# Performance work log

Measured on AMD Instinct MI355X. Metric: run time of the kernel, lower is better.

Reference implementation:

```python
import jax, jax.numpy as jnp
import numpy as np
import math

B, SQ, SK, DQ, DK = 16, 2048, 2048, 1024, 1024

def setup_inputs() -> dict:
    key = jax.random.key(0)
    ks = jax.random.split(key, 6)
    return {
        "bert_feature": jax.random.normal(ks[0], (B, SQ, DQ), dtype=jnp.float32),
        "knowledge_feature": jax.random.normal(ks[1], (B, SK, DK), dtype=jnp.float32),
        "w1_w": jax.random.normal(ks[2], (DK, DQ), dtype=jnp.float32) * 0.02,
        "w1_b": jax.random.normal(ks[3], (DK,), dtype=jnp.float32) * 0.02,
        "w2_w": jax.random.normal(ks[4], (DQ, DQ + DK), dtype=jnp.float32) * 0.02,
        "w2_b": jax.random.normal(ks[5], (DQ,), dtype=jnp.float32) * 0.02,
    }

def reference(bert_feature, knowledge_feature, w1_w, w1_b, w2_w, w2_b):
    d_k = knowledge_feature.shape[-1]
    # w1 projection: [B, Sq, d_q] -> [B, Sq, d_k]
    bf = jnp.einsum('bqd,kd->bqk', bert_feature, w1_w) + w1_b
    # scaled dot-product attention with knowledge as K and V
    scores = jnp.einsum('bqd,bkd->bqk', bf, knowledge_feature) / math.sqrt(d_k)
    attn = jax.nn.softmax(scores, axis=-1)
    output = jnp.einsum('bqk,bkd->bqd', attn, knowledge_feature)
    # concat + fusion linear: [B, Sq, d_q + d_k] -> [B, Sq, d_q]
    fused = jnp.concatenate([bert_feature, output], axis=-1)
    return jnp.einsum('bqf,of->bqo', fused, w2_w) + w2_b
```

## Files before the change

kernel.cpp:

```cpp
#include <hip/hip_runtime.h>

typedef __attribute__((ext_vector_type(8))) short s16x8;
typedef __attribute__((ext_vector_type(8))) unsigned short u16x8;
typedef __attribute__((ext_vector_type(4))) unsigned short u16x4;
typedef __attribute__((ext_vector_type(4))) float f32x4;

__device__ inline float bf2f(unsigned short h) {
  union { unsigned int u; float f; } x; x.u = ((unsigned int)h) << 16; return x.f;
}
__device__ inline unsigned short f2bf(float f) {
  union { float f; unsigned int u; } x; x.f = f;
  unsigned int u = x.u;
  return (unsigned short)((u + 0x7fffu + ((u >> 16) & 1u)) >> 16);
}

__global__ __launch_bounds__(256) void cvt_bf16(const float* __restrict__ in,
                                                unsigned short* __restrict__ out,
                                                long long n, int shift, int ldo) {
  long long i = (long long)blockIdx.x * 256 + threadIdx.x;
  long long stride = (long long)gridDim.x * 256;
  long long nchunks = n >> 3;
  for (; i < nchunks; i += stride) {
    long long e = i << 3;
    long long r = e >> shift;
    int c = (int)(e & ((1LL << shift) - 1));
    const float4* p = (const float4*)(in + e);
    float4 f0 = p[0], f1 = p[1];
    u16x8 u;
    u[0] = f2bf(f0.x); u[1] = f2bf(f0.y); u[2] = f2bf(f0.z); u[3] = f2bf(f0.w);
    u[4] = f2bf(f1.x); u[5] = f2bf(f1.y); u[6] = f2bf(f1.z); u[7] = f2bf(f1.w);
    *(u16x8*)&out[r * (long long)ldo + c] = u;
  }
}

__global__ __launch_bounds__(256) void transpose_bf16(const unsigned short* __restrict__ in,
                                                      unsigned short* __restrict__ out,
                                                      int rows, int cols) {
  __shared__ unsigned short tile[64][72];
  long long zoff = (long long)blockIdx.z * rows * cols;
  const unsigned short* src = in + zoff;
  unsigned short* dst = out + zoff;
  int k0 = blockIdx.x * 64, d0 = blockIdx.y * 64;
  int t = threadIdx.x;
  int rr = t >> 4;
  int cc = (t & 15) * 4;
#pragma unroll
  for (int i = 0; i < 4; ++i) {
    int k = rr + i * 16;
    u16x4 v = *(const u16x4*)&src[(long long)(k0 + k) * cols + d0 + cc];
    *(u16x4*)&tile[k][cc] = v;
  }
  __syncthreads();
#pragma unroll
  for (int i = 0; i < 4; ++i) {
    int d = rr + i * 16;
    u16x4 v;
#pragma unroll
    for (int j = 0; j < 4; ++j) v[j] = tile[cc + j][d];
    *(u16x4*)&dst[(long long)(d0 + d) * rows + k0 + cc] = v;
  }
}

__global__ __launch_bounds__(256) void softmax_rows(unsigned short* __restrict__ P) {
  int w = threadIdx.x >> 6, l = threadIdx.x & 63;
  long long row = (long long)blockIdx.x * 4 + w;
  unsigned short* p = P + row * 2048;
  float v[32];
  float m = -1e30f;
#pragma unroll
  for (int c = 0; c < 4; ++c) {
    u16x8 u = *(const u16x8*)&p[c * 512 + l * 8];
#pragma unroll
    for (int j = 0; j < 8; ++j) { v[c * 8 + j] = bf2f(u[j]); m = fmaxf(m, v[c * 8 + j]); }
  }
#pragma unroll
  for (int s = 32; s; s >>= 1) m = fmaxf(m, __shfl_xor(m, s));
  float sum = 0.f;
#pragma unroll
  for (int i = 0; i < 32; ++i) { v[i] = __expf(v[i] - m); sum += v[i]; }
#pragma unroll
  for (int s = 32; s; s >>= 1) sum += __shfl_xor(sum, s);
  float r = 1.0f / sum;
#pragma unroll
  for (int c = 0; c < 4; ++c) {
    u16x8 u;
#pragma unroll
    for (int j = 0; j < 8; ++j) u[j] = f2bf(v[c * 8 + j] * r);
    *(u16x8*)&p[c * 512 + l * 8] = u;
  }
}

template <bool OUT_BF16, bool HAS_BIAS>
__global__ __launch_bounds__(512, 1) void gemm256(
    const unsigned short* __restrict__ A, const unsigned short* __restrict__ Bt,
    void* __restrict__ C, const float* __restrict__ bias,
    int K, int lda, int ldb, int ldc,
    long long sA, long long sB, long long sC, float scale,
    int gx, int gy) {
  __shared__ char lds[131072];
  const int t = threadIdx.x;
  const int l = t & 63, w = t >> 6;
  const int wm = w >> 2, wn = w & 3;

  const int nwg = gridDim.x;
  const int id = blockIdx.x;
  const int sid = (id & 7) * (nwg >> 3) + (id >> 3);
  const int bx = sid % gx;
  const int rem = sid / gx;
  const int by = rem % gy;
  const int bz = rem / gy;

  A += (long long)bz * sA;
  Bt += (long long)bz * sB;
  const long long m0 = (long long)by * 256;
  const long long n0 = (long long)bx * 256;

  const int srow = t >> 2;
  const int sk = (((t & 3) * 16) ^ (((t >> 3) & 3) << 4)) >> 1;
  const unsigned short* ga0 = A + (m0 + srow) * lda + sk;
  const unsigned short* ga1 = A + (m0 + 128 + srow) * lda + sk;
  const unsigned short* gb0 = Bt + (n0 + srow) * ldb + sk;
  const unsigned short* gb1 = Bt + (n0 + 128 + srow) * ldb + sk;
  const int Lt = t * 16;

  const int laneoff = (l & 15) * 64 + ((((l >> 4) * 16)) ^ (((l >> 1) & 3) << 4));

  f32x4 acc[8][4] = {};
  const int nt = K >> 5;

#define STAGE_A(tt)                                                                  \
  {                                                                                  \
    char* s_ = lds + (((tt) & 3) * 32768);                                           \
    long long ko_ = (long long)(tt) * 32;                                            \
    __builtin_amdgcn_global_load_lds(                                                \
        (const __attribute__((address_space(1))) void*)(ga0 + ko_),                  \
        (__attribute__((address_space(3))) void*)(s_ + Lt), 16, 0, 0);               \
    __builtin_amdgcn_global_load_lds(                                                \
        (const __attribute__((address_space(1))) void*)(ga1 + ko_),                  \
        (__attribute__((address_space(3))) void*)(s_ + 8192 + Lt), 16, 0, 0);        \
  }
#define STAGE_B(tt)                                                                  \
  {                                                                                  \
    char* s_ = lds + (((tt) & 3) * 32768) + 16384;                                   \
    long long ko_ = (long long)(tt) * 32;                                            \
    __builtin_amdgcn_global_load_lds(                                                \
        (const __attribute__((address_space(1))) void*)(gb0 + ko_),                  \
        (__attribute__((address_space(3))) void*)(s_ + Lt), 16, 0, 0);               \
    __builtin_amdgcn_global_load_lds(                                                \
        (const __attribute__((address_space(1))) void*)(gb1 + ko_),                  \
        (__attribute__((address_space(3))) void*)(s_ + 8192 + Lt), 16, 0, 0);        \
  }

  STAGE_A(0); STAGE_B(0);
  STAGE_A(1); STAGE_B(1);
  STAGE_A(2); STAGE_B(2);
  asm volatile("s_waitcnt vmcnt(8)" ::: "memory");
  __builtin_amdgcn_s_barrier();

  for (int tt = 0; tt < nt; ++tt) {
    const char* sa = lds + ((tt & 3) * 32768) + wm * 8192;
    const char* sb = lds + ((tt & 3) * 32768) + 16384 + wn * 4096;
    s16x8 af[4], bf[4];
#pragma unroll
    for (int m = 0; m < 4; ++m) af[m] = *(const s16x8*)(sa + m * 1024 + laneoff);
#pragma unroll
    for (int n = 0; n < 4; ++n) bf[n] = *(const s16x8*)(sb + n * 1024 + laneoff);
    if (tt + 3 < nt) STAGE_A(tt + 3);
    __builtin_amdgcn_s_barrier();
    __builtin_amdgcn_s_setprio(1);
#pragma unroll
    for (int m = 0; m < 4; ++m)
#pragma unroll
      for (int n = 0; n < 4; ++n)
        acc[m][n] = __builtin_amdgcn_mfma_f32_16x16x32_bf16(af[m], bf[n], acc[m][n], 0, 0, 0);
    __builtin_amdgcn_s_setprio(0);
    __builtin_amdgcn_s_barrier();
#pragma unroll
    for (int m = 0; m < 4; ++m) af[m] = *(const s16x8*)(sa + (4 + m) * 1024 + laneoff);
    if (tt + 3 < nt) STAGE_B(tt + 3);
    __builtin_amdgcn_s_barrier();
    __builtin_amdgcn_s_setprio(1);
#pragma unroll
    for (int m = 0; m < 4; ++m)
#pragma unroll
      for (int n = 0; n < 4; ++n)
        acc[4 + m][n] = __builtin_amdgcn_mfma_f32_16x16x32_bf16(af[m], bf[n], acc[4 + m][n], 0, 0, 0);
    __builtin_amdgcn_s_setprio(0);
    const int ahead = nt - tt - 2;
    if (ahead >= 2)      asm volatile("s_waitcnt vmcnt(8)" ::: "memory");
    else if (ahead == 1) asm volatile("s_waitcnt vmcnt(4)" ::: "memory");
    else                 asm volatile("s_waitcnt vmcnt(0)" ::: "memory");
    __builtin_amdgcn_s_barrier();
  }
#undef STAGE_A
#undef STAGE_B

  const int cl = l & 15, rg = (l >> 4) * 4;
#pragma unroll
  for (int m = 0; m < 8; ++m) {
#pragma unroll
    for (int n = 0; n < 4; ++n) {
      long long col = n0 + wn * 64 + n * 16 + cl;
      long long row = m0 + wm * 128 + m * 16 + rg;
      float bb = HAS_BIAS ? bias[col] : 0.0f;
#pragma unroll
      for (int j = 0; j < 4; ++j) {
        float v = (acc[m][n][j] + bb) * scale;
        if (OUT_BF16)
          ((unsigned short*)C)[bz * sC + (row + j) * ldc + col] = f2bf(v);
        else
          ((float*)C)[bz * sC + (row + j) * ldc + col] = v;
      }
    }
  }
}

extern "C" void kernel_launch(void* const* d_in, const int* in_sizes, int n_in,
                              void* d_out, int out_size, void* d_ws, size_t ws_size,
                              hipStream_t stream) {
  const float* bert = (const float*)d_in[0];
  const float* know = (const float*)d_in[1];
  const float* w1w  = (const float*)d_in[2];
  const float* w1b  = (const float*)d_in[3];
  const float* w2w  = (const float*)d_in[4];
  const float* w2b  = (const float*)d_in[5];

  char* ws = (char*)d_ws;
  unsigned short* fused  = (unsigned short*)(ws);
  unsigned short* bfq    = (unsigned short*)(ws + 134217728LL);
  unsigned short* know16 = (unsigned short*)(ws + 201326592LL);
  unsigned short* knowT  = (unsigned short*)(ws + 268435456LL);
  unsigned short* w1_16  = (unsigned short*)(ws + 335544320LL);
  unsigned short* w2_16  = (unsigned short*)(ws + 337641472LL);
  unsigned short* P      = (unsigned short*)d_out;

  cvt_bf16<<<2048, 256, 0, stream>>>(bert, fused, 33554432LL, 10, 2048);
  cvt_bf16<<<2048, 256, 0, stream>>>(know, know16, 33554432LL, 10, 1024);
  cvt_bf16<<<512, 256, 0, stream>>>(w1w, w1_16, 1048576LL, 10, 1024);
  cvt_bf16<<<512, 256, 0, stream>>>(w2w, w2_16, 2097152LL, 11, 2048);
  transpose_bf16<<<dim3(32, 16, 16), 256, 0, stream>>>(know16, knowT, 2048, 1024);

  gemm256<true, true><<<4 * 128, 512, 0, stream>>>(
      fused, w1_16, bfq, w1b, 1024, 2048, 1024, 1024, 0, 0, 0, 0.03125f, 4, 128);

  gemm256<true, false><<<8 * 8 * 16, 512, 0, stream>>>(
      bfq, know16, P, nullptr, 1024, 1024, 1024, 2048,
      2048LL * 1024, 2048LL * 1024, 2048LL * 2048, 1.0f, 8, 8);

  softmax_rows<<<8192, 256, 0, stream>>>(P);

  gemm256<true, false><<<4 * 8 * 16, 512, 0, stream>>>(
      P, knowT, fused + 1024, nullptr, 2048, 2048, 2048, 2048,
      2048LL * 2048, 1024LL * 2048, 2048LL * 2048, 1.0f, 4, 8);

  gemm256<false, true><<<4 * 128, 512, 0, stream>>>(
      fused, w2_16, d_out, w2b, 2048, 2048, 2048, 1024, 0, 0, 0, 1.0f, 4, 128);
}
```

Measured before the change: 650.1 us.

## Double-buffer MFMA fragments in registers and cut per-tile barriers to one

Restructures the GEMM main loop so the next K-tile's A/B fragments are read from LDS into a second register set while the current tile's MFMAs run. The loop is unrolled by two with ping-pong fragment buffers. Global-to-LDS prefetch is issued at the start of each half, and the waitcnt/barrier pattern drops from three barriers per tile to one. This aims to hide LDS read latency and synchronisation stalls behind MFMA work, at the cost of more VGPRs and an assumption that the tile count is even.

```diff
diff --git a/kernel.cpp b/kernel.cpp
--- a/kernel.cpp
+++ b/kernel.cpp
@@ -154,44 +154,60 @@
   STAGE_A(0); STAGE_B(0);
   STAGE_A(1); STAGE_B(1);
   STAGE_A(2); STAGE_B(2);
-  asm volatile("s_waitcnt vmcnt(8)" ::: "memory");
+  asm volatile("s_waitcnt vmcnt(4)" ::: "memory");
   __builtin_amdgcn_s_barrier();
 
-  for (int tt = 0; tt < nt; ++tt) {
-    const char* sa = lds + ((tt & 3) * 32768) + wm * 8192;
-    const char* sb = lds + ((tt & 3) * 32768) + 16384 + wn * 4096;
-    s16x8 af[4], bf[4];
-#pragma unroll
-    for (int m = 0; m < 4; ++m) af[m] = *(const s16x8*)(sa + m * 1024 + laneoff);
-#pragma unroll
-    for (int n = 0; n < 4; ++n) bf[n] = *(const s16x8*)(sb + n * 1024 + laneoff);
-    if (tt + 3 < nt) STAGE_A(tt + 3);
-    __builtin_amdgcn_s_barrier();
-    __builtin_amdgcn_s_setprio(1);
-#pragma unroll
-    for (int m = 0; m < 4; ++m)
-#pragma unroll
-      for (int n = 0; n < 4; ++n)
-        acc[m][n] = __builtin_amdgcn_mfma_f32_16x16x32_bf16(af[m], bf[n], acc[m][n], 0, 0, 0);
-    __builtin_amdgcn_s_setprio(0);
-    __builtin_amdgcn_s_barrier();
-#pragma unroll
-    for (int m = 0; m < 4; ++m) af[m] = *(const s16x8*)(sa + (4 + m) * 1024 + laneoff);
-    if (tt + 3 < nt) STAGE_B(tt + 3);
-    __builtin_amdgcn_s_barrier();
-    __builtin_amdgcn_s_setprio(1);
-#pragma unroll
-    for (int m = 0; m < 4; ++m)
-#pragma unroll
-      for (int n = 0; n < 4; ++n)
-        acc[4 + m][n] = __builtin_amdgcn_mfma_f32_16x16x32_bf16(af[m], bf[n], acc[4 + m][n], 0, 0, 0);
-    __builtin_amdgcn_s_setprio(0);
-    const int ahead = nt - tt - 2;
-    if (ahead >= 2)      asm volatile("s_waitcnt vmcnt(8)" ::: "memory");
-    else if (ahead == 1) asm volatile("s_waitcnt vmcnt(4)" ::: "memory");
-    else                 asm volatile("s_waitcnt vmcnt(0)" ::: "memory");
-    __builtin_amdgcn_s_barrier();
-  }
+  s16x8 aA0[4], bA0[4], aA1[4], bA1[4];
+  {
+    const char* sa = lds + wm * 8192;
+    const char* sb = lds + 16384 + wn * 4096;
+#pragma unroll
+    for (int m = 0; m < 4; ++m) aA0[m] = *(const s16x8*)(sa + m * 1024 + laneoff);
+#pragma unroll
+    for (int n = 0; n < 4; ++n) bA0[n] = *(const s16x8*)(sb + n * 1024 + laneoff);
+  }
+
+#define HALF(TT, CA, CB, PA, PB)                                                     \
+  {                                                                                  \
+    const int tt_ = (TT);                                                            \
+    const char* sa_ = lds + ((tt_ & 3) * 32768) + wm * 8192;                         \
+    if (tt_ + 3 < nt) STAGE_A(tt_ + 3);                                              \
+    s16x8 fb_[4];                                                                    \
+    _Pragma("unroll")                                                                \
+    for (int m = 0; m < 4; ++m) fb_[m] = *(const s16x8*)(sa_ + (4 + m) * 1024 + laneoff); \
+    if (tt_ + 3 < nt) STAGE_B(tt_ + 3);                                              \
+    __builtin_amdgcn_s_setprio(1);                                                   \
+    _Pragma("unroll")                                                                \
+    for (int m = 0; m < 4; ++m)                                                      \
+      _Pragma("unroll")                                                              \
+      for (int n = 0; n < 4; ++n)                                                    \
+        acc[m][n] = __builtin_amdgcn_mfma_f32_16x16x32_bf16(CA[m], CB[n], acc[m][n], 0, 0, 0); \
+    __builtin_amdgcn_s_setprio(0);                                                   \
+    if (tt_ + 1 < nt) {                                                              \
+      const char* na_ = lds + (((tt_ + 1) & 3) * 32768) + wm * 8192;                 \
+      const char* nb_ = lds + (((tt_ + 1) & 3) * 32768) + 16384 + wn * 4096;         \
+      _Pragma("unroll")                                                              \
+      for (int m = 0; m < 4; ++m) PA[m] = *(const s16x8*)(na_ + m * 1024 + laneoff); \
+      _Pragma("unroll")                                                              \
+      for (int n = 0; n < 4; ++n) PB[n] = *(const s16x8*)(nb_ + n * 1024 + laneoff); \
+    }                                                                                \
+    __builtin_amdgcn_s_setprio(1);                                                   \
+    _Pragma("unroll")                                                                \
+    for (int m = 0; m < 4; ++m)                                                      \
+      _Pragma("unroll")                                                              \
+      for (int n = 0; n < 4; ++n)                                                    \
+        acc[4 + m][n] = __builtin_amdgcn_mfma_f32_16x16x32_bf16(fb_[m], CB[n], acc[4 + m][n], 0, 0, 0); \
+    __builtin_amdgcn_s_setprio(0);                                                   \
+    if (tt_ + 3 < nt) { asm volatile("s_waitcnt vmcnt(4)" ::: "memory"); }           \
+    else              { asm volatile("s_waitcnt vmcnt(0)" ::: "memory"); }           \
+    __builtin_amdgcn_s_barrier();                                                    \
+  }
+
+  for (int tt = 0; tt < nt; tt += 2) {
+    HALF(tt, aA0, bA0, aA1, bA1);
+    HALF(tt + 1, aA1, bA1, aA0, bA0);
+  }
+#undef HALF
 #undef STAGE_A
 #undef STAGE_B
 
```

Result: no change. 646.5 us (-0.6%).

## Restructure GEMM main loop to K=64 double-buffered tiles with finer staging

Applied to the files above, without the earlier changes.

The GEMM mainloop moves from a 4-stage ring of K=32 tiles to a 2-buffer scheme of K=64 tiles, each split into two K=32 slices. Global-to-LDS loads for the next tiles are interleaved across four MFMA quarters, with explicit lgkmcnt waits and barriers between them. The aim is fewer loop iterations and barrier rounds per unit of work and better overlap of loads with MFMA. The cost is more barriers per iteration and a more complex vmcnt accounting that could stall if miscounted. An unused pointer parameter was also added to the transpose kernel.

```diff
diff --git a/kernel.cpp b/kernel.cpp
--- a/kernel.cpp
+++ b/kernel.cpp
@@ -34,6 +34,7 @@
 }
 
 __global__ __launch_bounds__(256) void transpose_bf16(const unsigned short* __restrict__ in,
+                                                      const unsigned short* __restrict__ unused,
                                                       unsigned short* __restrict__ out,
                                                       int rows, int cols) {
   __shared__ unsigned short tile[64][72];
@@ -115,85 +116,93 @@
   const long long m0 = (long long)by * 256;
   const long long n0 = (long long)bx * 256;
 
-  const int srow = t >> 2;
-  const int sk = (((t & 3) * 16) ^ (((t >> 3) & 3) << 4)) >> 1;
-  const unsigned short* ga0 = A + (m0 + srow) * lda + sk;
-  const unsigned short* ga1 = A + (m0 + 128 + srow) * lda + sk;
-  const unsigned short* gb0 = Bt + (n0 + srow) * ldb + sk;
-  const unsigned short* gb1 = Bt + (n0 + 128 + srow) * ldb + sk;
+  const int trow = t >> 2;
+  const int kl8 = ((t & 3) ^ ((t >> 3) & 3)) * 8;
+  const unsigned short* gA = A + (m0 + trow) * lda + kl8;
+  const unsigned short* gB = Bt + (n0 + trow) * ldb + kl8;
   const int Lt = t * 16;
 
-  const int laneoff = (l & 15) * 64 + ((((l >> 4) * 16)) ^ (((l >> 1) & 3) << 4));
+  const int lo = (l & 15) * 64 + ((((l >> 4) ^ (((l & 15) >> 1) & 3))) << 4);
 
   f32x4 acc[8][4] = {};
-  const int nt = K >> 5;
-
-#define STAGE_A(tt)                                                                  \
+  const int nt = K >> 6;
+
+#define STAGE_A(KT, KSL)                                                             \
   {                                                                                  \
-    char* s_ = lds + (((tt) & 3) * 32768);                                           \
-    long long ko_ = (long long)(tt) * 32;                                            \
-    __builtin_amdgcn_global_load_lds(                                                \
-        (const __attribute__((address_space(1))) void*)(ga0 + ko_),                  \
-        (__attribute__((address_space(3))) void*)(s_ + Lt), 16, 0, 0);               \
-    __builtin_amdgcn_global_load_lds(                                                \
-        (const __attribute__((address_space(1))) void*)(ga1 + ko_),                  \
-        (__attribute__((address_space(3))) void*)(s_ + 8192 + Lt), 16, 0, 0);        \
-  }
-#define STAGE_B(tt)                                                                  \
+    char* d_ = lds + (((KT) & 1) * 65536) + ((KSL) * 16384);                         \
+    const unsigned short* g_ = gA + (long long)(KT) * 64 + (KSL) * 32;               \
+    __builtin_amdgcn_global_load_lds(                                                \
+        (const __attribute__((address_space(1))) void*)g_,                           \
+        (__attribute__((address_space(3))) void*)(d_ + Lt), 16, 0, 0);               \
+    __builtin_amdgcn_global_load_lds(                                                \
+        (const __attribute__((address_space(1))) void*)(g_ + 128 * lda),             \
+        (__attribute__((address_space(3))) void*)(d_ + 8192 + Lt), 16, 0, 0);        \
+  }
+#define STAGE_B(KT, KSL)                                                             \
   {                                                                                  \
-    char* s_ = lds + (((tt) & 3) * 32768) + 16384;                                   \
-    long long ko_ = (long long)(tt) * 32;                                            \
-    __builtin_amdgcn_global_load_lds(                                                \
-        (const __attribute__((address_space(1))) void*)(gb0 + ko_),                  \
-        (__attribute__((address_space(3))) void*)(s_ + Lt), 16, 0, 0);               \
-    __builtin_amdgcn_global_load_lds(                                                \
-        (const __attribute__((address_space(1))) void*)(gb1 + ko_),                  \
-        (__attribute__((address_space(3))) void*)(s_ + 8192 + Lt), 16, 0, 0);        \
-  }
-
-  STAGE_A(0); STAGE_B(0);
-  STAGE_A(1); STAGE_B(1);
-  STAGE_A(2); STAGE_B(2);
-  asm volatile("s_waitcnt vmcnt(8)" ::: "memory");
+    char* d_ = lds + (((KT) & 1) * 65536) + 32768 + ((KSL) * 16384);                 \
+    const unsigned short* g_ = gB + (long long)(KT) * 64 + (KSL) * 32;               \
+    __builtin_amdgcn_global_load_lds(                                                \
+        (const __attribute__((address_space(1))) void*)g_,                           \
+        (__attribute__((address_space(3))) void*)(d_ + Lt), 16, 0, 0);               \
+    __builtin_amdgcn_global_load_lds(                                                \
+        (const __attribute__((address_space(1))) void*)(g_ + 128 * ldb),             \
+        (__attribute__((address_space(3))) void*)(d_ + 8192 + Lt), 16, 0, 0);        \
+  }
+
+  STAGE_A(0, 0); STAGE_A(0, 1); STAGE_B(0, 0); STAGE_B(0, 1);
+  STAGE_B(1, 0); STAGE_A(1, 0); STAGE_B(1, 1);
+  asm volatile("s_waitcnt vmcnt(6)" ::: "memory");
   __builtin_amdgcn_s_barrier();
 
-  for (int tt = 0; tt < nt; ++tt) {
-    const char* sa = lds + ((tt & 3) * 32768) + wm * 8192;
-    const char* sb = lds + ((tt & 3) * 32768) + 16384 + wn * 4096;
-    s16x8 af[4], bf[4];
-#pragma unroll
-    for (int m = 0; m < 4; ++m) af[m] = *(const s16x8*)(sa + m * 1024 + laneoff);
-#pragma unroll
-    for (int n = 0; n < 4; ++n) bf[n] = *(const s16x8*)(sb + n * 1024 + laneoff);
-    if (tt + 3 < nt) STAGE_A(tt + 3);
-    __builtin_amdgcn_s_barrier();
-    __builtin_amdgcn_s_setprio(1);
-#pragma unroll
-    for (int m = 0; m < 4; ++m)
-#pragma unroll
-      for (int n = 0; n < 4; ++n)
-        acc[m][n] = __builtin_amdgcn_mfma_f32_16x16x32_bf16(af[m], bf[n], acc[m][n], 0, 0, 0);
-    __builtin_amdgcn_s_setprio(0);
-    __builtin_amdgcn_s_barrier();
-#pragma unroll
-    for (int m = 0; m < 4; ++m) af[m] = *(const s16x8*)(sa + (4 + m) * 1024 + laneoff);
-    if (tt + 3 < nt) STAGE_B(tt + 3);
-    __builtin_amdgcn_s_barrier();
-    __builtin_amdgcn_s_setprio(1);
-#pragma unroll
-    for (int m = 0; m < 4; ++m)
-#pragma unroll
-      for (int n = 0; n < 4; ++n)
-        acc[4 + m][n] = __builtin_amdgcn_mfma_f32_16x16x32_bf16(af[m], bf[n], acc[4 + m][n], 0, 0, 0);
-    __builtin_amdgcn_s_setprio(0);
-    const int ahead = nt - tt - 2;
-    if (ahead >= 2)      asm volatile("s_waitcnt vmcnt(8)" ::: "memory");
-    else if (ahead == 1) asm volatile("s_waitcnt vmcnt(4)" ::: "memory");
-    else                 asm volatile("s_waitcnt vmcnt(0)" ::: "memory");
-    __builtin_amdgcn_s_barrier();
+  s16x8 af[4], bf[4];
+
+#define READ_A(MH, KSL, CB)                                                          \
+  _Pragma("unroll")                                                                  \
+  for (int m_ = 0; m_ < 4; ++m_)                                                     \
+    af[m_] = *(const s16x8*)((CB) + (KSL) * 16384 + wm * 8192 + ((MH) * 4 + m_) * 1024 + lo);
+#define READ_B(KSL, CB)                                                              \
+  _Pragma("unroll")                                                                  \
+  for (int n_ = 0; n_ < 4; ++n_)                                                     \
+    bf[n_] = *(const s16x8*)((CB) + 32768 + (KSL) * 16384 + wn * 4096 + n_ * 1024 + lo);
+#define MFMA_Q(MH)                                                                   \
+  __builtin_amdgcn_s_setprio(1);                                                     \
+  _Pragma("unroll")                                                                  \
+  for (int m_ = 0; m_ < 4; ++m_)                                                     \
+    _Pragma("unroll")                                                                \
+    for (int n_ = 0; n_ < 4; ++n_)                                                   \
+      acc[(MH) * 4 + m_][n_] =                                                       \
+          __builtin_amdgcn_mfma_f32_16x16x32_bf16(af[m_], bf[n_], acc[(MH) * 4 + m_][n_], 0, 0, 0); \
+  __builtin_amdgcn_s_setprio(0);
+#define BAR __builtin_amdgcn_s_barrier()
+#define LGKM0 asm volatile("s_waitcnt lgkmcnt(0)" ::: "memory")
+
+  for (int kt = 0; kt < nt; ++kt) {
+    const char* cb = lds + (kt & 1) * 65536;
+    const bool p1 = (kt + 1 < nt), p2 = (kt + 2 < nt);
+    READ_B(0, cb); READ_A(0, 0, cb);
+    if (p1) STAGE_A(kt + 1, 1);
+    BAR; LGKM0; MFMA_Q(0); BAR;
+    READ_A(1, 0, cb);
+    if (p2) STAGE_B(kt + 2, 0);
+    BAR; LGKM0; MFMA_Q(1); BAR;
+    READ_B(1, cb); READ_A(0, 1, cb);
+    if (p2) STAGE_A(kt + 2, 0);
+    BAR; LGKM0; MFMA_Q(0); BAR;
+    READ_A(1, 1, cb);
+    if (p2) STAGE_B(kt + 2, 1);
+    BAR; LGKM0; MFMA_Q(1);
+    if (p2)      asm volatile("s_waitcnt vmcnt(6)" ::: "memory");
+    else         asm volatile("s_waitcnt vmcnt(0)" ::: "memory");
+    BAR;
   }
 #undef STAGE_A
 #undef STAGE_B
+#undef READ_A
+#undef READ_B
+#undef MFMA_Q
+#undef BAR
+#undef LGKM0
 
   const int cl = l & 15, rg = (l >> 4) * 4;
 #pragma unroll
@@ -238,7 +247,7 @@
   cvt_bf16<<<2048, 256, 0, stream>>>(know, know16, 33554432LL, 10, 1024);
   cvt_bf16<<<512, 256, 0, stream>>>(w1w, w1_16, 1048576LL, 10, 1024);
   cvt_bf16<<<512, 256, 0, stream>>>(w2w, w2_16, 2097152LL, 11, 2048);
-  transpose_bf16<<<dim3(32, 16, 16), 256, 0, stream>>>(know16, knowT, 2048, 1024);
+  transpose_bf16<<<dim3(32, 16, 16), 256, 0, stream>>>(know16, nullptr, knowT, 2048, 1024);
 
   gemm256<true, true><<<4 * 128, 512, 0, stream>>>(
       fused, w1_16, bfq, w1b, 1024, 2048, 1024, 1024, 0, 0, 0, 0.03125f, 4, 128);
```

Result: no change. 645.6 us (-0.7%).
